# Kernel tuning notes

Hardware: AMD Instinct MI355X
Metric: run time of the kernel (lower is better)

Reference implementation:

```python
import jax, jax.numpy as jnp
import numpy as np

E = 8      # num_experts
D = 1024   # input_size
H = 1024   # hidden_size
K = 2      # top_k
B = 2
S = 1024


def setup_inputs() -> dict:
    key = jax.random.key(0)
    ks = jax.random.split(key, 5)
    x = jax.random.normal(ks[0], (B, S, D), dtype=jnp.float32)
    p = jax.random.uniform(ks[1], (B * S, K), dtype=jnp.float32)
    expert_p = p / p.sum(axis=-1, keepdims=True)            # normalized top-k gates
    expert_idxs = jax.random.randint(ks[2], (B * S, K), 0, E)
    W1 = jax.random.normal(ks[3], (E, D, 2 * H), dtype=jnp.float32) * (D ** -0.5)
    W2 = jax.random.normal(ks[4], (E, H, D), dtype=jnp.float32) * (H ** -0.5)
    return {"x": x, "expert_p": expert_p, "expert_idxs": expert_idxs, "W1": W1, "W2": W2}


def reference(x, expert_p, expert_idxs, W1, W2):
    x_shape = x.shape
    xf = x.reshape(-1, x_shape[-1])                 # [N, D]
    n_tok = xf.shape[0]
    k = expert_idxs.shape[-1]
    x_pair = jnp.repeat(xf, k, axis=0)              # [N*K, D] token replicated per expert slot
    idx = expert_idxs.reshape(-1)                   # [N*K]
    p = expert_p.reshape(-1)                        # [N*K]
    y_pair = jnp.zeros((n_tok * k, x_shape[-1]), dtype=x.dtype)
    # loop over fixed small expert count; masked dense GEMM per expert
    for e in range(W1.shape[0]):
        m = (idx == e).astype(x.dtype)[:, None]     # [N*K, 1]
        hg = (x_pair * m) @ W1[e]                   # [N*K, 2H]
        h, g = jnp.split(hg, 2, axis=-1)            # chunk(2): (h, gates)
        a = jax.nn.silu(g) * h                      # SiLU-gated GLU
        y_pair = y_pair + (a @ W2[e]) * m           # [N*K, D]
    # combine: weight each pair by its gate prob and sum over top_k slots
    y = (y_pair * p[:, None]).reshape(n_tok, k, -1).sum(axis=1)
    return y.reshape(x_shape)
```

## Files before the change

### kernel.cpp

```cpp
#include <hip/hip_runtime.h>


typedef __bf16 bf16x8 __attribute__((ext_vector_type(8)));
typedef __bf16 bf16x4 __attribute__((ext_vector_type(4)));
typedef float  f32x4  __attribute__((ext_vector_type(4)));

#define NPAIR 4096
#define NTOK  2048
#define DDIM  1024
#define HDIM  1024
#define NEXP  8

#define ORDER_I   64
#define XB_OFF    (24576)
#define W1T_OFF   (XB_OFF + 4194304)
#define W2T_OFF   (W1T_OFF + 33554432)
#define ACT_OFF   (W2T_OFF + 16777216)
#define YP_OFF    (ACT_OFF + 10485760)

#define GLOAD_LDS16(g, l) \
    __builtin_amdgcn_global_load_lds( \
        (const __attribute__((address_space(1))) void*)(g), \
        (__attribute__((address_space(3))) void*)(l), 16, 0, 0)

__global__ void bucket_kernel(const int* __restrict__ idx, int* __restrict__ wsi) {
    __shared__ int cnt[NEXP], base[NEXP], cur[NEXP];
    const int t = threadIdx.x;
    if (t < NEXP) { cnt[t] = 0; cur[t] = 0; }
    __syncthreads();
    for (int i = t; i < NPAIR; i += 256) atomicAdd(&cnt[idx[i] & 7], 1);
    __syncthreads();
    if (t == 0) {
        int off = 0;
        for (int e = 0; e < NEXP; e++) {
            base[e] = off;
            wsi[e] = cnt[e];
            wsi[8 + e] = off;
            off += (cnt[e] + 127) & ~127;
        }
    }
    __syncthreads();
    for (int i = t; i < 5120; i += 256) wsi[ORDER_I + i] = 0;
    __syncthreads();
    for (int i = t; i < NPAIR; i += 256) {
        int e = idx[i] & 7;
        int s = atomicAdd(&cur[e], 1);
        wsi[ORDER_I + base[e] + s] = i;
    }
}

__global__ void cvtx_kernel(const float* __restrict__ x, __bf16* __restrict__ xb) {
    int i = (blockIdx.x * 256 + threadIdx.x) * 4;
    float4 v = *(const float4*)(x + i);
    bf16x4 o;
    o[0] = (__bf16)v.x; o[1] = (__bf16)v.y; o[2] = (__bf16)v.z; o[3] = (__bf16)v.w;
    *(bf16x4*)(xb + i) = o;
}

__global__ __launch_bounds__(256) void tcvt_kernel(const float* __restrict__ src,
                                                   __bf16* __restrict__ dst,
                                                   int R, int C) {
    __shared__ float t[64][65];
    const int tid = threadIdx.x;
    const float* s = src + (size_t)blockIdx.z * R * C;
    __bf16* d = dst + (size_t)blockIdx.z * R * C;
    const int r0 = blockIdx.y * 64, c0 = blockIdx.x * 64;
    const int lr = tid >> 4;
    const int lc = (tid & 15) * 4;
#pragma unroll
    for (int p = 0; p < 4; p++) {
        int r = p * 16 + lr;
        float4 v = *(const float4*)(s + (size_t)(r0 + r) * C + c0 + lc);
        t[r][lc] = v.x; t[r][lc + 1] = v.y; t[r][lc + 2] = v.z; t[r][lc + 3] = v.w;
    }
    __syncthreads();
#pragma unroll
    for (int p = 0; p < 4; p++) {
        int c = p * 16 + lr;
        bf16x4 o;
#pragma unroll
        for (int i = 0; i < 4; i++) o[i] = (__bf16)t[lc + i][c];
        *(bf16x4*)(d + (size_t)(c0 + c) * R + r0 + lc) = o;
    }
}

__global__ __launch_bounds__(256) void gemm1_kernel(const __bf16* __restrict__ xb,
                                                    const __bf16* __restrict__ w1t,
                                                    const int* __restrict__ wsi,
                                                    __bf16* __restrict__ act) {
    const int e = blockIdx.z;
    const int cnt = wsi[e];
    const int m0 = blockIdx.y * 128;
    if (m0 >= cnt) return;
    const int base = wsi[8 + e];
    const int n0 = blockIdx.x * 64;
    const int* order = wsi + ORDER_I;
    const __bf16* w1e = w1t + (size_t)e * 2048 * 1024;

    __shared__ __align__(16) __bf16 As[128][32];
    __shared__ __align__(16) __bf16 Bs[128][32];

    const int tid = threadIdx.x;
    const int lane = tid & 63, w = tid >> 6;
    const int lm = lane & 15, q = lane >> 4;
    const int wm = w & 1, wn = w >> 1;

    const __bf16* ga[2];
    const __bf16* gb[2];
#pragma unroll
    for (int j = 0; j < 2; j++) {
        int c = j * 256 + tid;
        int r = c >> 2, ks = (c & 3) * 8;
        int m = m0 + r; if (m >= cnt) m = cnt - 1;
        int tok = order[base + m] >> 1;
        ga[j] = xb + (size_t)tok * DDIM + ks;
        int half = r >> 6, rr = r & 63;
        int rb = (rr < 32) ? (n0 + half * 32 + rr)
                           : (HDIM + n0 + half * 32 + (rr - 32));
        gb[j] = w1e + (size_t)rb * DDIM + ks;
    }

    f32x4 acc[4][4];
#pragma unroll
    for (int mt = 0; mt < 4; mt++)
#pragma unroll
        for (int nt = 0; nt < 4; nt++) acc[mt][nt] = (f32x4){0.f, 0.f, 0.f, 0.f};

    for (int k0 = 0; k0 < DDIM; k0 += 32) {
        __syncthreads();
#pragma unroll
        for (int j = 0; j < 2; j++) {
            int c = j * 256 + tid;
            GLOAD_LDS16(ga[j], (char*)&As[0][0] + c * 16);
            GLOAD_LDS16(gb[j], (char*)&Bs[0][0] + c * 16);
            ga[j] += 32; gb[j] += 32;
        }
        __syncthreads();
        bf16x8 af[4];
#pragma unroll
        for (int mt = 0; mt < 4; mt++)
            af[mt] = *(const bf16x8*)(&As[wm * 64 + mt * 16 + lm][q * 8]);
#pragma unroll
        for (int nt = 0; nt < 4; nt++) {
            bf16x8 b = *(const bf16x8*)(&Bs[wn * 64 + nt * 16 + lm][q * 8]);
#pragma unroll
            for (int mt = 0; mt < 4; mt++)
                acc[mt][nt] = __builtin_amdgcn_mfma_f32_16x16x32_bf16(af[mt], b, acc[mt][nt], 0, 0, 0);
        }
    }

#pragma unroll
    for (int mt = 0; mt < 4; mt++) {
        int mbase = m0 + wm * 64 + mt * 16 + q * 4;
#pragma unroll
        for (int ntp = 0; ntp < 2; ntp++) {
            int col = n0 + wn * 32 + ntp * 16 + lm;
#pragma unroll
            for (int r = 0; r < 4; r++) {
                int m = mbase + r;
                if (m < cnt) {
                    float h = acc[mt][ntp][r];
                    float g = acc[mt][ntp + 2][r];
                    float a = h * (g / (1.f + __expf(-g)));
                    act[(size_t)(base + m) * HDIM + col] = (__bf16)a;
                }
            }
        }
    }
}

__global__ __launch_bounds__(256) void gemm2_kernel(const __bf16* __restrict__ act,
                                                    const __bf16* __restrict__ w2t,
                                                    const int* __restrict__ wsi,
                                                    float* __restrict__ yp) {
    const int e = blockIdx.z;
    const int cnt = wsi[e];
    const int m0 = blockIdx.y * 128;
    if (m0 >= cnt) return;
    const int base = wsi[8 + e];
    const int n0 = blockIdx.x * 128;
    const int* order = wsi + ORDER_I;
    const __bf16* w2e = w2t + (size_t)e * 1024 * 1024;

    __shared__ __align__(16) __bf16 As[128][32];
    __shared__ __align__(16) __bf16 Bs[128][32];

    const int tid = threadIdx.x;
    const int lane = tid & 63, w = tid >> 6;
    const int lm = lane & 15, q = lane >> 4;
    const int wm = w & 1, wn = w >> 1;

    const __bf16* ga[2];
    const __bf16* gb[2];
#pragma unroll
    for (int j = 0; j < 2; j++) {
        int c = j * 256 + tid;
        int r = c >> 2, ks = (c & 3) * 8;
        ga[j] = act + (size_t)(base + m0 + r) * HDIM + ks;
        gb[j] = w2e + (size_t)(n0 + r) * HDIM + ks;
    }

    f32x4 acc[4][4];
#pragma unroll
    for (int mt = 0; mt < 4; mt++)
#pragma unroll
        for (int nt = 0; nt < 4; nt++) acc[mt][nt] = (f32x4){0.f, 0.f, 0.f, 0.f};

    for (int k0 = 0; k0 < HDIM; k0 += 32) {
        __syncthreads();
#pragma unroll
        for (int j = 0; j < 2; j++) {
            int c = j * 256 + tid;
            GLOAD_LDS16(ga[j], (char*)&As[0][0] + c * 16);
            GLOAD_LDS16(gb[j], (char*)&Bs[0][0] + c * 16);
            ga[j] += 32; gb[j] += 32;
        }
        __syncthreads();
        bf16x8 af[4];
#pragma unroll
        for (int mt = 0; mt < 4; mt++)
            af[mt] = *(const bf16x8*)(&As[wm * 64 + mt * 16 + lm][q * 8]);
#pragma unroll
        for (int nt = 0; nt < 4; nt++) {
            bf16x8 b = *(const bf16x8*)(&Bs[wn * 64 + nt * 16 + lm][q * 8]);
#pragma unroll
            for (int mt = 0; mt < 4; mt++)
                acc[mt][nt] = __builtin_amdgcn_mfma_f32_16x16x32_bf16(af[mt], b, acc[mt][nt], 0, 0, 0);
        }
    }

    int pi[4][4];
#pragma unroll
    for (int mt = 0; mt < 4; mt++)
#pragma unroll
        for (int r = 0; r < 4; r++) {
            int gm = m0 + wm * 64 + mt * 16 + q * 4 + r;
            pi[mt][r] = (gm < cnt) ? order[base + gm] : -1;
        }
#pragma unroll
    for (int mt = 0; mt < 4; mt++)
#pragma unroll
        for (int nt = 0; nt < 4; nt++) {
            int col = n0 + wn * 64 + nt * 16 + lm;
#pragma unroll
            for (int r = 0; r < 4; r++) {
                if (pi[mt][r] >= 0)
                    yp[(size_t)pi[mt][r] * DDIM + col] = acc[mt][nt][r];
            }
        }
}

__global__ void combine_kernel(const float* __restrict__ yp, const float* __restrict__ p,
                               float* __restrict__ out) {
    int id = blockIdx.x * 256 + threadIdx.x;
    int n = id >> 8;
    int c = (id & 255) << 2;
    const float4 v0 = *(const float4*)(yp + (size_t)(2 * n) * DDIM + c);
    const float4 v1 = *(const float4*)(yp + (size_t)(2 * n + 1) * DDIM + c);
    float p0 = p[2 * n], p1 = p[2 * n + 1];
    float4 o;
    o.x = p0 * v0.x + p1 * v1.x;
    o.y = p0 * v0.y + p1 * v1.y;
    o.z = p0 * v0.z + p1 * v1.z;
    o.w = p0 * v0.w + p1 * v1.w;
    *(float4*)(out + (size_t)n * DDIM + c) = o;
}

extern "C" void kernel_launch(void* const* d_in, const int* in_sizes, int n_in,
                              void* d_out, int out_size, void* d_ws, size_t ws_size,
                              hipStream_t stream) {
    (void)in_sizes; (void)n_in; (void)out_size; (void)ws_size;
    const float* x   = (const float*)d_in[0];
    const float* p   = (const float*)d_in[1];
    const int* eidx  = (const int*)d_in[2];
    const float* W1  = (const float*)d_in[3];
    const float* W2  = (const float*)d_in[4];
    float* out = (float*)d_out;

    char* ws = (char*)d_ws;
    int* wsi     = (int*)ws;
    __bf16* xb   = (__bf16*)(ws + XB_OFF);
    __bf16* w1t  = (__bf16*)(ws + W1T_OFF);
    __bf16* w2t  = (__bf16*)(ws + W2T_OFF);
    __bf16* act  = (__bf16*)(ws + ACT_OFF);
    float* yp    = (float*)(ws + YP_OFF);

    bucket_kernel<<<1, 256, 0, stream>>>(eidx, wsi);
    cvtx_kernel<<<(NTOK * DDIM) / (256 * 4), 256, 0, stream>>>(x, xb);
    tcvt_kernel<<<dim3(32, 16, NEXP), 256, 0, stream>>>(W1, w1t, DDIM, 2 * HDIM);
    tcvt_kernel<<<dim3(16, 16, NEXP), 256, 0, stream>>>(W2, w2t, HDIM, DDIM);
    gemm1_kernel<<<dim3(16, 32, NEXP), 256, 0, stream>>>(xb, w1t, wsi, act);
    gemm2_kernel<<<dim3(8, 32, NEXP), 256, 0, stream>>>(act, w2t, wsi, yp);
    combine_kernel<<<NTOK, 256, 0, stream>>>(yp, p, out);
}
```

Baseline: 227.0 us.

## Merge prep kernels, widen GEMM K-tiles, fuse combine into gemm2 via atomics

Folds the bucketing, x conversion, both weight transposes and zeroing of the output into one launch. Both GEMMs now stage K=64 per iteration instead of 32, which halves the number of barriers. gemm2 uses 64-wide N tiles and scatters gate-weighted results straight into the output with float atomicAdd, so the yp buffer and the combine kernel go away. The atomics add contention and make the summation order nondeterministic. The zeroing of the order array's padding was also dropped.

```diff
diff --git a/kernel.cpp b/kernel.cpp
--- a/kernel.cpp
+++ b/kernel.cpp
@@ -16,55 +16,16 @@
 #define W1T_OFF   (XB_OFF + 4194304)
 #define W2T_OFF   (W1T_OFF + 33554432)
 #define ACT_OFF   (W2T_OFF + 16777216)
-#define YP_OFF    (ACT_OFF + 10485760)
 
 #define GLOAD_LDS16(g, l) \
     __builtin_amdgcn_global_load_lds( \
         (const __attribute__((address_space(1))) void*)(g), \
         (__attribute__((address_space(3))) void*)(l), 16, 0, 0)
 
-__global__ void bucket_kernel(const int* __restrict__ idx, int* __restrict__ wsi) {
-    __shared__ int cnt[NEXP], base[NEXP], cur[NEXP];
-    const int t = threadIdx.x;
-    if (t < NEXP) { cnt[t] = 0; cur[t] = 0; }
-    __syncthreads();
-    for (int i = t; i < NPAIR; i += 256) atomicAdd(&cnt[idx[i] & 7], 1);
-    __syncthreads();
-    if (t == 0) {
-        int off = 0;
-        for (int e = 0; e < NEXP; e++) {
-            base[e] = off;
-            wsi[e] = cnt[e];
-            wsi[8 + e] = off;
-            off += (cnt[e] + 127) & ~127;
-        }
-    }
-    __syncthreads();
-    for (int i = t; i < 5120; i += 256) wsi[ORDER_I + i] = 0;
-    __syncthreads();
-    for (int i = t; i < NPAIR; i += 256) {
-        int e = idx[i] & 7;
-        int s = atomicAdd(&cur[e], 1);
-        wsi[ORDER_I + base[e] + s] = i;
-    }
-}
-
-__global__ void cvtx_kernel(const float* __restrict__ x, __bf16* __restrict__ xb) {
-    int i = (blockIdx.x * 256 + threadIdx.x) * 4;
-    float4 v = *(const float4*)(x + i);
-    bf16x4 o;
-    o[0] = (__bf16)v.x; o[1] = (__bf16)v.y; o[2] = (__bf16)v.z; o[3] = (__bf16)v.w;
-    *(bf16x4*)(xb + i) = o;
-}
-
-__global__ __launch_bounds__(256) void tcvt_kernel(const float* __restrict__ src,
-                                                   __bf16* __restrict__ dst,
-                                                   int R, int C) {
-    __shared__ float t[64][65];
-    const int tid = threadIdx.x;
-    const float* s = src + (size_t)blockIdx.z * R * C;
-    __bf16* d = dst + (size_t)blockIdx.z * R * C;
-    const int r0 = blockIdx.y * 64, c0 = blockIdx.x * 64;
+__device__ __forceinline__ void tcvt_tile(const float* __restrict__ s,
+                                          __bf16* __restrict__ d,
+                                          int R, int C, int r0, int c0,
+                                          float (*t)[65], int tid) {
     const int lr = tid >> 4;
     const int lc = (tid & 15) * 4;
 #pragma unroll
@@ -81,6 +42,65 @@
 #pragma unroll
         for (int i = 0; i < 4; i++) o[i] = (__bf16)t[lc + i][c];
         *(bf16x4*)(d + (size_t)(c0 + c) * R + r0 + lc) = o;
+    }
+}
+
+__global__ __launch_bounds__(256) void prep_kernel(const float* __restrict__ x,
+                                                   const float* __restrict__ W1,
+                                                   const float* __restrict__ W2,
+                                                   const int* __restrict__ idx,
+                                                   int* __restrict__ wsi,
+                                                   __bf16* __restrict__ xb,
+                                                   __bf16* __restrict__ w1t,
+                                                   __bf16* __restrict__ w2t,
+                                                   float* __restrict__ out) {
+    __shared__ float t[64][65];
+    __shared__ int cnt[NEXP], base[NEXP], cur[NEXP];
+    const int b = blockIdx.x;
+    const int tid = threadIdx.x;
+    if (b < 4096) {
+        int e = b >> 9, tt = b & 511;
+        int c0 = (tt & 31) * 64, r0 = (tt >> 5) * 64;
+        tcvt_tile(W1 + (size_t)e * DDIM * 2 * HDIM, w1t + (size_t)e * 2 * HDIM * DDIM,
+                  DDIM, 2 * HDIM, r0, c0, t, tid);
+    } else if (b < 6144) {
+        int b2 = b - 4096;
+        int e = b2 >> 8, tt = b2 & 255;
+        int c0 = (tt & 15) * 64, r0 = (tt >> 4) * 64;
+        tcvt_tile(W2 + (size_t)e * HDIM * DDIM, w2t + (size_t)e * DDIM * HDIM,
+                  HDIM, DDIM, r0, c0, t, tid);
+    } else if (b < 8192) {
+        int i = (b - 6144) * 1024 + tid * 4;
+        float4 v = *(const float4*)(x + i);
+        bf16x4 o;
+        o[0] = (__bf16)v.x; o[1] = (__bf16)v.y; o[2] = (__bf16)v.z; o[3] = (__bf16)v.w;
+        *(bf16x4*)(xb + i) = o;
+    } else if (b < 8704) {
+        int base4 = (b - 8192) * 4096;
+        float4 z = {0.f, 0.f, 0.f, 0.f};
+#pragma unroll
+        for (int j = 0; j < 4; j++)
+            *(float4*)(out + base4 + j * 1024 + tid * 4) = z;
+    } else {
+        if (tid < NEXP) { cnt[tid] = 0; cur[tid] = 0; }
+        __syncthreads();
+        for (int i = tid; i < NPAIR; i += 256) atomicAdd(&cnt[idx[i] & 7], 1);
+        __syncthreads();
+        if (tid == 0) {
+            int off = 0;
+            for (int e = 0; e < NEXP; e++) {
+                base[e] = off;
+                wsi[e] = cnt[e];
+                wsi[8 + e] = off;
+                off += (cnt[e] + 127) & ~127;
+            }
+        }
+        __syncthreads();
+        for (int i = tid; i < NPAIR; i += 256) {
+            int e = idx[i] & 7;
+            int s = atomicAdd(&cur[e], 1);
+            wsi[ORDER_I + base[e] + s] = i;
+        }
     }
 }
 
@@ -97,20 +117,20 @@
     const int* order = wsi + ORDER_I;
     const __bf16* w1e = w1t + (size_t)e * 2048 * 1024;
 
-    __shared__ __align__(16) __bf16 As[128][32];
-    __shared__ __align__(16) __bf16 Bs[128][32];
+    __shared__ __align__(16) __bf16 As[128][64];
+    __shared__ __align__(16) __bf16 Bs[128][64];
 
     const int tid = threadIdx.x;
     const int lane = tid & 63, w = tid >> 6;
     const int lm = lane & 15, q = lane >> 4;
     const int wm = w & 1, wn = w >> 1;
 
-    const __bf16* ga[2];
-    const __bf16* gb[2];
-#pragma unroll
-    for (int j = 0; j < 2; j++) {
+    const __bf16* ga[4];
+    const __bf16* gb[4];
+#pragma unroll
+    for (int j = 0; j < 4; j++) {
         int c = j * 256 + tid;
-        int r = c >> 2, ks = (c & 3) * 8;
+        int r = c >> 3, ks = (c & 7) * 8;
         int m = m0 + r; if (m >= cnt) m = cnt - 1;
         int tok = order[base + m] >> 1;
         ga[j] = xb + (size_t)tok * DDIM + ks;
@@ -126,26 +146,29 @@
 #pragma unroll
         for (int nt = 0; nt < 4; nt++) acc[mt][nt] = (f32x4){0.f, 0.f, 0.f, 0.f};
 
-    for (int k0 = 0; k0 < DDIM; k0 += 32) {
-        __syncthreads();
-#pragma unroll
-        for (int j = 0; j < 2; j++) {
+    for (int k0 = 0; k0 < DDIM; k0 += 64) {
+        __syncthreads();
+#pragma unroll
+        for (int j = 0; j < 4; j++) {
             int c = j * 256 + tid;
             GLOAD_LDS16(ga[j], (char*)&As[0][0] + c * 16);
             GLOAD_LDS16(gb[j], (char*)&Bs[0][0] + c * 16);
-            ga[j] += 32; gb[j] += 32;
-        }
-        __syncthreads();
-        bf16x8 af[4];
-#pragma unroll
-        for (int mt = 0; mt < 4; mt++)
-            af[mt] = *(const bf16x8*)(&As[wm * 64 + mt * 16 + lm][q * 8]);
-#pragma unroll
-        for (int nt = 0; nt < 4; nt++) {
-            bf16x8 b = *(const bf16x8*)(&Bs[wn * 64 + nt * 16 + lm][q * 8]);
+            ga[j] += 64; gb[j] += 64;
+        }
+        __syncthreads();
+#pragma unroll
+        for (int kh = 0; kh < 2; kh++) {
+            bf16x8 af[4];
 #pragma unroll
             for (int mt = 0; mt < 4; mt++)
-                acc[mt][nt] = __builtin_amdgcn_mfma_f32_16x16x32_bf16(af[mt], b, acc[mt][nt], 0, 0, 0);
+                af[mt] = *(const bf16x8*)(&As[wm * 64 + mt * 16 + lm][kh * 32 + q * 8]);
+#pragma unroll
+            for (int nt = 0; nt < 4; nt++) {
+                bf16x8 bfr = *(const bf16x8*)(&Bs[wn * 64 + nt * 16 + lm][kh * 32 + q * 8]);
+#pragma unroll
+                for (int mt = 0; mt < 4; mt++)
+                    acc[mt][nt] = __builtin_amdgcn_mfma_f32_16x16x32_bf16(af[mt], bfr, acc[mt][nt], 0, 0, 0);
+            }
         }
     }
 
@@ -172,98 +195,103 @@
 __global__ __launch_bounds__(256) void gemm2_kernel(const __bf16* __restrict__ act,
                                                     const __bf16* __restrict__ w2t,
                                                     const int* __restrict__ wsi,
-                                                    float* __restrict__ yp) {
+                                                    const float* __restrict__ p,
+                                                    float* __restrict__ out) {
     const int e = blockIdx.z;
     const int cnt = wsi[e];
     const int m0 = blockIdx.y * 128;
     if (m0 >= cnt) return;
     const int base = wsi[8 + e];
-    const int n0 = blockIdx.x * 128;
+    const int n0 = blockIdx.x * 64;
     const int* order = wsi + ORDER_I;
     const __bf16* w2e = w2t + (size_t)e * 1024 * 1024;
 
-    __shared__ __align__(16) __bf16 As[128][32];
-    __shared__ __align__(16) __bf16 Bs[128][32];
+    __shared__ __align__(16) __bf16 As[128][64];
+    __shared__ __align__(16) __bf16 Bs[64][64];
 
     const int tid = threadIdx.x;
     const int lane = tid & 63, w = tid >> 6;
     const int lm = lane & 15, q = lane >> 4;
     const int wm = w & 1, wn = w >> 1;
 
-    const __bf16* ga[2];
+    const __bf16* ga[4];
     const __bf16* gb[2];
+#pragma unroll
+    for (int j = 0; j < 4; j++) {
+        int c = j * 256 + tid;
+        int r = c >> 3, ks = (c & 7) * 8;
+        ga[j] = act + (size_t)(base + m0 + r) * HDIM + ks;
+    }
 #pragma unroll
     for (int j = 0; j < 2; j++) {
         int c = j * 256 + tid;
-        int r = c >> 2, ks = (c & 3) * 8;
-        ga[j] = act + (size_t)(base + m0 + r) * HDIM + ks;
+        int r = c >> 3, ks = (c & 7) * 8;
         gb[j] = w2e + (size_t)(n0 + r) * HDIM + ks;
     }
 
-    f32x4 acc[4][4];
+    f32x4 acc[4][2];
 #pragma unroll
     for (int mt = 0; mt < 4; mt++)
 #pragma unroll
-        for (int nt = 0; nt < 4; nt++) acc[mt][nt] = (f32x4){0.f, 0.f, 0.f, 0.f};
-
-    for (int k0 = 0; k0 < HDIM; k0 += 32) {
-        __syncthreads();
+        for (int nt = 0; nt < 2; nt++) acc[mt][nt] = (f32x4){0.f, 0.f, 0.f, 0.f};
+
+    for (int k0 = 0; k0 < HDIM; k0 += 64) {
+        __syncthreads();
+#pragma unroll
+        for (int j = 0; j < 4; j++) {
+            int c = j * 256 + tid;
+            GLOAD_LDS16(ga[j], (char*)&As[0][0] + c * 16);
+            ga[j] += 64;
+        }
 #pragma unroll
         for (int j = 0; j < 2; j++) {
             int c = j * 256 + tid;
-            GLOAD_LDS16(ga[j], (char*)&As[0][0] + c * 16);
             GLOAD_LDS16(gb[j], (char*)&Bs[0][0] + c * 16);
-            ga[j] += 32; gb[j] += 32;
-        }
-        __syncthreads();
-        bf16x8 af[4];
-#pragma unroll
-        for (int mt = 0; mt < 4; mt++)
-            af[mt] = *(const bf16x8*)(&As[wm * 64 + mt * 16 + lm][q * 8]);
-#pragma unroll
-        for (int nt = 0; nt < 4; nt++) {
-            bf16x8 b = *(const bf16x8*)(&Bs[wn * 64 + nt * 16 + lm][q * 8]);
+            gb[j] += 64;
+        }
+        __syncthreads();
+#pragma unroll
+        for (int kh = 0; kh < 2; kh++) {
+            bf16x8 af[4];
 #pragma unroll
             for (int mt = 0; mt < 4; mt++)
-                acc[mt][nt] = __builtin_amdgcn_mfma_f32_16x16x32_bf16(af[mt], b, acc[mt][nt], 0, 0, 0);
+                af[mt] = *(const bf16x8*)(&As[wm * 64 + mt * 16 + lm][kh * 32 + q * 8]);
+#pragma unroll
+            for (int nt = 0; nt < 2; nt++) {
+                bf16x8 bfr = *(const bf16x8*)(&Bs[wn * 32 + nt * 16 + lm][kh * 32 + q * 8]);
+#pragma unroll
+                for (int mt = 0; mt < 4; mt++)
+                    acc[mt][nt] = __builtin_amdgcn_mfma_f32_16x16x32_bf16(af[mt], bfr, acc[mt][nt], 0, 0, 0);
+            }
         }
     }
 
     int pi[4][4];
+    float pw[4][4];
 #pragma unroll
     for (int mt = 0; mt < 4; mt++)
 #pragma unroll
         for (int r = 0; r < 4; r++) {
             int gm = m0 + wm * 64 + mt * 16 + q * 4 + r;
-            pi[mt][r] = (gm < cnt) ? order[base + gm] : -1;
+            if (gm < cnt) {
+                int pr = order[base + gm];
+                pi[mt][r] = pr;
+                pw[mt][r] = p[pr];
+            } else pi[mt][r] = -1;
         }
 #pragma unroll
     for (int mt = 0; mt < 4; mt++)
 #pragma unroll
-        for (int nt = 0; nt < 4; nt++) {
-            int col = n0 + wn * 64 + nt * 16 + lm;
+        for (int nt = 0; nt < 2; nt++) {
+            int col = n0 + wn * 32 + nt * 16 + lm;
 #pragma unroll
             for (int r = 0; r < 4; r++) {
-                if (pi[mt][r] >= 0)
-                    yp[(size_t)pi[mt][r] * DDIM + col] = acc[mt][nt][r];
-            }
-        }
-}
-
-__global__ void combine_kernel(const float* __restrict__ yp, const float* __restrict__ p,
-                               float* __restrict__ out) {
-    int id = blockIdx.x * 256 + threadIdx.x;
-    int n = id >> 8;
-    int c = (id & 255) << 2;
-    const float4 v0 = *(const float4*)(yp + (size_t)(2 * n) * DDIM + c);
-    const float4 v1 = *(const float4*)(yp + (size_t)(2 * n + 1) * DDIM + c);
-    float p0 = p[2 * n], p1 = p[2 * n + 1];
-    float4 o;
-    o.x = p0 * v0.x + p1 * v1.x;
-    o.y = p0 * v0.y + p1 * v1.y;
-    o.z = p0 * v0.z + p1 * v1.z;
-    o.w = p0 * v0.w + p1 * v1.w;
-    *(float4*)(out + (size_t)n * DDIM + c) = o;
+                if (pi[mt][r] >= 0) {
+                    int tok = pi[mt][r] >> 1;
+                    atomicAdd(out + (size_t)tok * DDIM + col, pw[mt][r] * acc[mt][nt][r]);
+                }
+            }
+        }
 }
 
 extern "C" void kernel_launch(void* const* d_in, const int* in_sizes, int n_in,
@@ -283,13 +311,8 @@
     __bf16* w1t  = (__bf16*)(ws + W1T_OFF);
     __bf16* w2t  = (__bf16*)(ws + W2T_OFF);
     __bf16* act  = (__bf16*)(ws + ACT_OFF);
-    float* yp    = (float*)(ws + YP_OFF);
-
-    bucket_kernel<<<1, 256, 0, stream>>>(eidx, wsi);
-    cvtx_kernel<<<(NTOK * DDIM) / (256 * 4), 256, 0, stream>>>(x, xb);
-    tcvt_kernel<<<dim3(32, 16, NEXP), 256, 0, stream>>>(W1, w1t, DDIM, 2 * HDIM);
-    tcvt_kernel<<<dim3(16, 16, NEXP), 256, 0, stream>>>(W2, w2t, HDIM, DDIM);
+
+    prep_kernel<<<8705, 256, 0, stream>>>(x, W1, W2, eidx, wsi, xb, w1t, w2t, out);
     gemm1_kernel<<<dim3(16, 32, NEXP), 256, 0, stream>>>(xb, w1t, wsi, act);
-    gemm2_kernel<<<dim3(8, 32, NEXP), 256, 0, stream>>>(act, w2t, wsi, yp);
-    combine_kernel<<<NTOK, 256, 0, stream>>>(yp, p, out);
-}
+    gemm2_kernel<<<dim3(16, 32, NEXP), 256, 0, stream>>>(act, w2t, wsi, p, out);
+}
```

Result: slower. 235.5 us (+3.7%).
